# Kernel tuning notes

Hardware: AMD Instinct MI355X
Metric: run time of the kernel (lower is better)

## Reference

```python
import jax, jax.numpy as jnp
import numpy as np

E = 1024
H = 16
D = E // H
NUM_BUCKETS = 320
MAX_DISTANCE = 800


def _relative_positions_bucket(relative_positions):
    # relative_positions: int32 [T, S]
    num_buckets = NUM_BUCKETS // 2  # 160
    relative_buckets = (relative_positions > 0).astype(jnp.int32) * num_buckets
    rel = jnp.abs(relative_positions)
    max_exact = num_buckets // 2  # 80
    is_small = rel < max_exact
    rel_f = jnp.maximum(rel, 1).astype(jnp.float32)
    large = jnp.log(rel_f / max_exact) / np.log(MAX_DISTANCE / max_exact) * (num_buckets - max_exact)
    large = (max_exact + large).astype(jnp.int32)
    large = jnp.minimum(large, num_buckets - 1)
    relative_buckets = relative_buckets + jnp.where(is_small, rel, large)
    return relative_buckets


def setup_inputs() -> dict:
    key = jax.random.key(0)
    ks = jax.random.split(key, 12)
    B, T = 2, 2048
    s = 0.02
    return {
        "hidden_states": jax.random.normal(ks[0], (B, T, E), dtype=jnp.float32),
        "q_w": jax.random.normal(ks[1], (E, E), dtype=jnp.float32) * s,
        "q_b": jnp.zeros((E,), dtype=jnp.float32),
        "k_w": jax.random.normal(ks[2], (E, E), dtype=jnp.float32) * s,
        "k_b": jnp.zeros((E,), dtype=jnp.float32),
        "v_w": jax.random.normal(ks[3], (E, E), dtype=jnp.float32) * s,
        "v_b": jnp.zeros((E,), dtype=jnp.float32),
        "out_w": jax.random.normal(ks[4], (E, E), dtype=jnp.float32) * s,
        "out_b": jnp.zeros((E,), dtype=jnp.float32),
        "rel_embed": jax.random.normal(ks[5], (NUM_BUCKETS, H), dtype=jnp.float32) * s,
        "gru_const": jnp.ones((1, H, 1, 1), dtype=jnp.float32),
        "gru_w": jax.random.normal(ks[6], (8, D), dtype=jnp.float32) * s,
        "gru_b": jnp.zeros((8,), dtype=jnp.float32),
    }


def reference(hidden_states, q_w, q_b, k_w, k_b, v_w, v_b, out_w, out_b,
              rel_embed, gru_const, gru_w, gru_b):
    B, T, _ = hidden_states.shape
    scaling = D ** (-0.5)

    # --- relative position bias: [H, T, T] ---
    ctx = jnp.arange(T, dtype=jnp.int32)[:, None]
    mem = jnp.arange(T, dtype=jnp.int32)[None, :]
    buckets = _relative_positions_bucket(mem - ctx)          # [T, T]
    position_bias = rel_embed[buckets]                        # [T, T, H]
    position_bias = jnp.transpose(position_bias, (2, 0, 1))   # [H, T, T]

    # --- gate (gru_rel_pos): per (b, h, t) scalar ---
    gated = hidden_states.reshape(B, T, H, D).transpose(0, 2, 1, 3)  # [B,H,T,D]
    proj = jnp.einsum('bhtd,ed->bhte', gated, gru_w) + gru_b         # [B,H,T,8]
    proj = proj.reshape(B, H, T, 2, 4).sum(-1)                        # [B,H,T,2]
    gate = jax.nn.sigmoid(proj)
    gate_a = gate[..., 0:1]
    gate_b = gate[..., 1:2]
    gate_out = gate_a * (gate_b * gru_const - 1.0) + 2.0              # [B,H,T,1]
    gated_position_bias = gate_out * position_bias[None]              # [B,H,T,T]

    # --- attention (same math as F.multi_head_attention_forward eager path) ---
    q = (hidden_states @ q_w.T + q_b).reshape(B, T, H, D).transpose(0, 2, 1, 3) * scaling
    k = (hidden_states @ k_w.T + k_b).reshape(B, T, H, D).transpose(0, 2, 1, 3)
    v = (hidden_states @ v_w.T + v_b).reshape(B, T, H, D).transpose(0, 2, 1, 3)

    scores = jnp.einsum('bhtd,bhsd->bhts', q, k) + gated_position_bias
    attn = jax.nn.softmax(scores, axis=-1)
    ctx_out = jnp.einsum('bhts,bhsd->bhtd', attn, v)                  # [B,H,T,D]
    ctx_out = ctx_out.transpose(0, 2, 1, 3).reshape(B, T, E)
    return ctx_out @ out_w.T + out_b
```

## Files before the change

### kernel.cpp

```cpp
#include <hip/hip_runtime.h>
#include <hip/hip_bf16.h>
#include <math.h>

typedef __bf16 bf16;
typedef __bf16 bf16x4 __attribute__((ext_vector_type(4)));
typedef __bf16 bf16x8 __attribute__((ext_vector_type(8)));
typedef float  f32x4  __attribute__((ext_vector_type(4)));

#define T_SEQ 2048
#define E_DIM 1024
#define H_NUM 16
#define D_DIM 64
#define NDELTA 4095
#define LOG2E 1.4426950408889634f

__device__ __forceinline__ void gld16(const bf16* g, bf16* l) {
  __builtin_amdgcn_global_load_lds((__attribute__((address_space(1))) void*)(g),
                                   (__attribute__((address_space(3))) void*)(l), 16, 0, 0);
}

__global__ void cast_bf16_kernel(const float* __restrict__ src, bf16* __restrict__ dst, int n4) {
  int i = blockIdx.x * blockDim.x + threadIdx.x;
  if (i >= n4) return;
  const float4 v = reinterpret_cast<const float4*>(src)[i];
  bf16x4 o;
  o[0] = (bf16)v.x; o[1] = (bf16)v.y; o[2] = (bf16)v.z; o[3] = (bf16)v.w;
  reinterpret_cast<bf16x4*>(dst)[i] = o;
}

__global__ void cast_w_kernel(const float* __restrict__ q_w, const float* __restrict__ k_w,
                              const float* __restrict__ v_w, const float* __restrict__ o_w,
                              bf16* __restrict__ wcat, bf16* __restrict__ wob) {
  int i = blockIdx.x * 256 + threadIdx.x;
  int sel = blockIdx.y;
  const float* src = (sel == 0) ? q_w : (sel == 1) ? k_w : (sel == 2) ? v_w : o_w;
  bf16* dst = (sel < 3) ? (wcat + (size_t)sel * 1048576) : wob;
  const float4 v = reinterpret_cast<const float4*>(src)[i];
  bf16x4 o;
  o[0] = (bf16)v.x; o[1] = (bf16)v.y; o[2] = (bf16)v.z; o[3] = (bf16)v.w;
  reinterpret_cast<bf16x4*>(dst)[i] = o;
}

__global__ void pb_kernel(const float* __restrict__ rel_embed, float* __restrict__ pbt) {
  int dd = blockIdx.x * 64 + threadIdx.x;
  if (dd >= NDELTA) return;
  int delta = dd - (T_SEQ - 1);
  int bucket = (delta > 0) ? 160 : 0;
  int rel = abs(delta);
  int v;
  if (rel < 80) {
    v = rel;
  } else {
    float rf = (float)(rel < 1 ? 1 : rel);
    float lf = logf(rf / 80.0f) * (80.0f / 2.302585092994046f);
    int lg = 80 + (int)lf;
    v = lg < 159 ? lg : 159;
  }
  bucket += v;
#pragma unroll
  for (int h = 0; h < H_NUM; h++)
    pbt[h * NDELTA + dd] = rel_embed[bucket * H_NUM + h];
}

__global__ __launch_bounds__(256)
void gate_kernel(const float* __restrict__ hs, const float* __restrict__ gru_w,
                 const float* __restrict__ gru_b, const float* __restrict__ gconst,
                 float* __restrict__ gate)
{
  __shared__ float w[512];
  int tid = threadIdx.x;
  w[tid] = gru_w[tid];
  w[tid + 256] = gru_w[tid + 256];
  __syncthreads();
  int idx = blockIdx.x * 256 + tid;
  int h  = idx & 15;
  int bt = idx >> 4;
  const float* x = hs + (size_t)bt * E_DIM + h * D_DIM;
  float acc[8] = {0,0,0,0,0,0,0,0};
  for (int d = 0; d < 64; d += 4) {
    float4 xv = *(const float4*)&x[d];
#pragma unroll
    for (int e = 0; e < 8; e++) {
      acc[e] += xv.x * w[e*64+d] + xv.y * w[e*64+d+1]
              + xv.z * w[e*64+d+2] + xv.w * w[e*64+d+3];
    }
  }
  float p0 = acc[0]+acc[1]+acc[2]+acc[3] + gru_b[0]+gru_b[1]+gru_b[2]+gru_b[3];
  float p1 = acc[4]+acc[5]+acc[6]+acc[7] + gru_b[4]+gru_b[5]+gru_b[6]+gru_b[7];
  float ga = 1.0f / (1.0f + expf(-p0));
  float gb = 1.0f / (1.0f + expf(-p1));
  float g = (ga * (gb * gconst[h] - 1.0f) + 2.0f) * LOG2E;
  int bb = bt >> 11;
  int t  = bt & (T_SEQ - 1);
  gate[((size_t)(bb * H_NUM + h)) * T_SEQ + t] = g;
}

template<int MODE, int BM, int BN>
__global__ __launch_bounds__(256, 4)
void gemm4_kernel(const bf16* __restrict__ A, const bf16* __restrict__ W,
                  const float* __restrict__ b0, const float* __restrict__ b1,
                  const float* __restrict__ b2, float qalpha,
                  void* __restrict__ out0, void* __restrict__ out1, void* __restrict__ out2)
{
  constexpr int AM = BM / 32;
  constexpr int AN = BN / 32;
  __shared__ bf16 As[2][BM * 32];
  __shared__ bf16 Bs[2][BN * 32];
  const int tid  = threadIdx.x;
  const int lane = tid & 63;
  const int wave = tid >> 6;
  const int m0 = blockIdx.y * BM;
  const int n0 = blockIdx.x * BN;
  const int wm = (wave >> 1) * (BM / 2);
  const int wn = (wave & 1) * (BN / 2);
  const int qd = lane >> 4;
  const int lm = lane & 15;

  const int row4 = lane >> 2;
  const int col8 = (lane & 3) * 8;
  const bf16* gA0 = A + (size_t)(m0 + wave * (BM / 4) + row4) * 1024 + col8;
  const bf16* gB0 = W + (size_t)(n0 + wave * (BN / 4) + row4) * 1024 + col8;
  bf16* lA = (bf16*)As + wave * (BM / 4) * 32;
  bf16* lB = (bf16*)Bs + wave * (BN / 4) * 32;

  gld16(gA0, lA);
  if (BM == 128) gld16(gA0 + (size_t)16 * 1024, lA + 512);
  gld16(gB0, lB);
  if (BN == 128) gld16(gB0 + (size_t)16 * 1024, lB + 512);
  __syncthreads();

  f32x4 acc[AM][AN] = {};

  for (int k0 = 0; k0 < 1024; k0 += 32) {
    const int buf = (k0 >> 5) & 1;
    if (k0 + 32 < 1024) {
      bf16* lA1 = lA + (buf ^ 1) * (BM * 32);
      bf16* lB1 = lB + (buf ^ 1) * (BN * 32);
      gld16(gA0 + k0 + 32, lA1);
      if (BM == 128) gld16(gA0 + (size_t)16 * 1024 + k0 + 32, lA1 + 512);
      gld16(gB0 + k0 + 32, lB1);
      if (BN == 128) gld16(gB0 + (size_t)16 * 1024 + k0 + 32, lB1 + 512);
    }
    bf16x8 af[AM], bfr[AN];
#pragma unroll
    for (int i = 0; i < AM; i++)
      af[i]  = *(const bf16x8*)&As[buf][(wm + i * 16 + lm) * 32 + qd * 8];
#pragma unroll
    for (int i = 0; i < AN; i++)
      bfr[i] = *(const bf16x8*)&Bs[buf][(wn + i * 16 + lm) * 32 + qd * 8];
#pragma unroll
    for (int im = 0; im < AM; im++)
#pragma unroll
      for (int in = 0; in < AN; in++)
        acc[im][in] = __builtin_amdgcn_mfma_f32_16x16x32_bf16(af[im], bfr[in], acc[im][in], 0, 0, 0);
    __syncthreads();
  }

  const int seg = n0 >> 10;
  const float* bias = (MODE == 0) ? b0 : (seg == 0 ? b0 : (seg == 1 ? b1 : b2));
  const float alpha = (MODE == 1 && seg == 0) ? qalpha : 1.0f;

#pragma unroll
  for (int im = 0; im < AM; im++) {
#pragma unroll
    for (int in = 0; in < AN; in++) {
      const int n  = n0 + wn + in * 16 + lm;
      const int n1 = n & 1023;
      const float bv = bias[n1];
      const int mb = m0 + wm + im * 16 + qd * 4;
      if (MODE == 0) {
        float* o = (float*)out0;
#pragma unroll
        for (int r = 0; r < 4; r++)
          o[(size_t)(mb + r) * 1024 + n1] = acc[im][in][r] + bv;
      } else if (seg == 2) {
        const int bb = mb >> 11;
        const int t  = mb & 2047;
        bf16x4 pk;
#pragma unroll
        for (int r = 0; r < 4; r++) pk[r] = (bf16)(acc[im][in][r] + bv);
        *(bf16x4*)&((bf16*)out2)[((size_t)(bb * 1024 + n1)) * 2048 + t] = pk;
      } else {
        bf16* o = (bf16*)(seg == 0 ? out0 : out1);
#pragma unroll
        for (int r = 0; r < 4; r++)
          o[(size_t)(mb + r) * 1024 + n1] = (bf16)((acc[im][in][r] + bv) * alpha);
      }
    }
  }
}

#define LK 72
__global__ __launch_bounds__(256)
void attn3_kernel(const bf16* __restrict__ Qg, const bf16* __restrict__ Kg,
                  const bf16* __restrict__ Vtg, const float* __restrict__ gate,
                  const float* __restrict__ pbt, bf16* __restrict__ ctx)
{
  __shared__ bf16 Ks[2][64 * LK];
  __shared__ bf16 Vs[2][64 * LK];
  __shared__ bf16 Ps[4][32 * LK];
  __shared__ float pbs[2176];

  const int t0 = blockIdx.x * 128;
  const int h  = blockIdx.y;
  const int b  = blockIdx.z;
  const int tid  = threadIdx.x;
  const int lane = tid & 63;
  const int wave = tid >> 6;
  const int qd = lane >> 4;
  const int lm = lane & 15;

  for (int i = tid; i < 2176; i += 256) {
    int idx = i - t0 + 1920;
    pbs[i] = (idx >= 0 && idx < NDELTA) ? pbt[h * NDELTA + idx] : 0.0f;
  }

  bf16x8 qf[2][2];
  float g[2];
#pragma unroll
  for (int nb = 0; nb < 2; nb++) {
    const int q = t0 + wave * 32 + nb * 16 + lm;
    const bf16* qrow = Qg + (size_t)(b * T_SEQ + q) * E_DIM + h * D_DIM;
    qf[nb][0] = *(const bf16x8*)(qrow + qd * 8);
    qf[nb][1] = *(const bf16x8*)(qrow + 32 + qd * 8);
    g[nb] = gate[((size_t)(b * H_NUM + h)) * T_SEQ + q];
  }

  const int srow = tid >> 2;
  const int scol = (tid & 3) * 16;
  const bf16* kgp = Kg  + ((size_t)(b * T_SEQ) + srow) * E_DIM + h * D_DIM + scol;
  const bf16* vgp = Vtg + ((size_t)(b * 1024) + h * D_DIM + srow) * T_SEQ + scol;

  {
    bf16x8 a0 = *(const bf16x8*)kgp;
    bf16x8 a1 = *(const bf16x8*)(kgp + 8);
    bf16x8 c0 = *(const bf16x8*)vgp;
    bf16x8 c1 = *(const bf16x8*)(vgp + 8);
    *(bf16x8*)&Ks[0][srow * LK + scol]     = a0;
    *(bf16x8*)&Ks[0][srow * LK + scol + 8] = a1;
    *(bf16x8*)&Vs[0][srow * LK + scol]     = c0;
    *(bf16x8*)&Vs[0][srow * LK + scol + 8] = c1;
  }
  __syncthreads();

  f32x4 o[4][2] = {};
  float li[2] = {0.0f, 0.0f};
  bf16* psw = &Ps[wave][0];

  for (int it = 0; it < T_SEQ / 64; it++) {
    const int s0 = it * 64;
    const int buf = it & 1;
    const bool more = (it + 1 < T_SEQ / 64);
    bf16x8 nk0, nk1, nv0, nv1;
    if (more) {
      const bf16* kn = kgp + (size_t)(s0 + 64) * E_DIM;
      const bf16* vn = vgp + (s0 + 64);
      nk0 = *(const bf16x8*)kn; nk1 = *(const bf16x8*)(kn + 8);
      nv0 = *(const bf16x8*)vn; nv1 = *(const bf16x8*)(vn + 8);
    }

    bf16x8 kf[4][2];
#pragma unroll
    for (int mb = 0; mb < 4; mb++) {
      kf[mb][0] = *(const bf16x8*)&Ks[buf][(16 * mb + lm) * LK + qd * 8];
      kf[mb][1] = *(const bf16x8*)&Ks[buf][(16 * mb + lm) * LK + 32 + qd * 8];
    }
#pragma unroll
    for (int nb = 0; nb < 2; nb++) {
      f32x4 sc[4];
#pragma unroll
      for (int mb = 0; mb < 4; mb++) {
        f32x4 t = {};
        t = __builtin_amdgcn_mfma_f32_16x16x32_bf16(kf[mb][0], qf[nb][0], t, 0, 0, 0);
        t = __builtin_amdgcn_mfma_f32_16x16x32_bf16(kf[mb][1], qf[nb][1], t, 0, 0, 0);
        sc[mb] = t;
      }
      const int ib = s0 + 4 * qd + 127 - (wave * 32 + nb * 16 + lm);
      float rs = 0.0f;
#pragma unroll
      for (int mb = 0; mb < 4; mb++) {
        bf16x4 pk;
#pragma unroll
        for (int r = 0; r < 4; r++) {
          float p = __builtin_amdgcn_exp2f(sc[mb][r] + g[nb] * pbs[ib + 16 * mb + r]);
          rs += p;
          pk[r] = (bf16)p;
        }
        *(bf16x4*)&psw[(nb * 16 + lm) * LK + 16 * mb + 4 * qd] = pk;
      }
      li[nb] += rs;
    }
    bf16x8 pf[2][2];
#pragma unroll
    for (int nb = 0; nb < 2; nb++) {
      pf[nb][0] = *(const bf16x8*)&psw[(nb * 16 + lm) * LK + qd * 8];
      pf[nb][1] = *(const bf16x8*)&psw[(nb * 16 + lm) * LK + 32 + qd * 8];
    }
#pragma unroll
    for (int db = 0; db < 4; db++) {
      bf16x8 vf0 = *(const bf16x8*)&Vs[buf][(16 * db + lm) * LK + qd * 8];
      bf16x8 vf1 = *(const bf16x8*)&Vs[buf][(16 * db + lm) * LK + 32 + qd * 8];
#pragma unroll
      for (int nb = 0; nb < 2; nb++) {
        o[db][nb] = __builtin_amdgcn_mfma_f32_16x16x32_bf16(vf0, pf[nb][0], o[db][nb], 0, 0, 0);
        o[db][nb] = __builtin_amdgcn_mfma_f32_16x16x32_bf16(vf1, pf[nb][1], o[db][nb], 0, 0, 0);
      }
    }
    if (more) {
      *(bf16x8*)&Ks[buf ^ 1][srow * LK + scol]     = nk0;
      *(bf16x8*)&Ks[buf ^ 1][srow * LK + scol + 8] = nk1;
      *(bf16x8*)&Vs[buf ^ 1][srow * LK + scol]     = nv0;
      *(bf16x8*)&Vs[buf ^ 1][srow * LK + scol + 8] = nv1;
    }
    __syncthreads();
  }

#pragma unroll
  for (int nb = 0; nb < 2; nb++) {
    li[nb] += __shfl_xor(li[nb], 16);
    li[nb] += __shfl_xor(li[nb], 32);
  }
#pragma unroll
  for (int nb = 0; nb < 2; nb++) {
    const float inv = 1.0f / li[nb];
    const int q = t0 + wave * 32 + nb * 16 + lm;
    bf16* obase = ctx + (size_t)(b * T_SEQ + q) * E_DIM + h * D_DIM + 4 * qd;
#pragma unroll
    for (int db = 0; db < 4; db++) {
      bf16x4 ov;
      ov[0] = (bf16)(o[db][nb][0] * inv); ov[1] = (bf16)(o[db][nb][1] * inv);
      ov[2] = (bf16)(o[db][nb][2] * inv); ov[3] = (bf16)(o[db][nb][3] * inv);
      *(bf16x4*)&obase[16 * db] = ov;
    }
  }
}

extern "C" void kernel_launch(void* const* d_in, const int* in_sizes, int n_in,
                              void* d_out, int out_size, void* d_ws, size_t ws_size,
                              hipStream_t stream)
{
  const float* hs     = (const float*)d_in[0];
  const float* q_w    = (const float*)d_in[1];
  const float* q_b    = (const float*)d_in[2];
  const float* k_w    = (const float*)d_in[3];
  const float* k_b    = (const float*)d_in[4];
  const float* v_w    = (const float*)d_in[5];
  const float* v_b    = (const float*)d_in[6];
  const float* out_w  = (const float*)d_in[7];
  const float* out_b  = (const float*)d_in[8];
  const float* rel    = (const float*)d_in[9];
  const float* gconst = (const float*)d_in[10];
  const float* gru_w  = (const float*)d_in[11];
  const float* gru_b  = (const float*)d_in[12];

  char* p = (char*)d_ws;
  bf16* hsb  = (bf16*)p; p += (size_t)4096 * 1024 * 2;
  bf16* wcat = (bf16*)p; p += (size_t)3072 * 1024 * 2;
  bf16* wob  = (bf16*)p; p += (size_t)1024 * 1024 * 2;
  bf16* Qb   = (bf16*)p; p += (size_t)4096 * 1024 * 2;
  bf16* Kb   = (bf16*)p; p += (size_t)4096 * 1024 * 2;
  bf16* Vtb  = (bf16*)p; p += (size_t)2048 * 2048 * 2;
  bf16* ctxb = (bf16*)p; p += (size_t)4096 * 1024 * 2;
  float* gatep = (float*)p; p += (size_t)2 * H_NUM * T_SEQ * 4;
  float* pbt   = (float*)p; p += (size_t)H_NUM * NDELTA * 4;

  cast_bf16_kernel<<<4096, 256, 0, stream>>>(hs, hsb, 1048576);
  cast_w_kernel<<<dim3(1024, 4), 256, 0, stream>>>(q_w, k_w, v_w, out_w, wcat, wob);
  pb_kernel<<<64, 64, 0, stream>>>(rel, pbt);
  gate_kernel<<<256, 256, 0, stream>>>(hs, gru_w, gru_b, gconst, gatep);

  const float qalpha = 0.125f * LOG2E;
  gemm4_kernel<1, 64, 128><<<dim3(24, 64), 256, 0, stream>>>(
      hsb, wcat, q_b, k_b, v_b, qalpha, Qb, Kb, Vtb);

  attn3_kernel<<<dim3(T_SEQ / 128, H_NUM, 2), 256, 0, stream>>>(Qb, Kb, Vtb, gatep, pbt, ctxb);

  gemm4_kernel<0, 64, 64><<<dim3(16, 64), 256, 0, stream>>>(
      ctxb, wob, out_b, nullptr, nullptr, 1.0f, d_out, nullptr, nullptr);
}
```

Before: 229.9 us.

## Fuse prep kernels into one launch and rework attention bias and K/V buffering

Merges the four preprocessing kernels (input cast, weight cast, position-bias table, gate) into a single launch that dispatches on block index, removing three kernel launches. The attention kernel now stores the position bias as four shifted bf16 copies so each lane reads an aligned bf16x4 vector instead of four scalar floats. It also drops K/V double buffering in favour of a single buffer with two barriers per iteration, which cuts LDS use but serialises the refill against compute. The bf16 bias storage adds a small rounding error.

```diff
diff --git a/kernel.cpp b/kernel.cpp
--- a/kernel.cpp
+++ b/kernel.cpp
@@ -19,80 +19,82 @@
                                    (__attribute__((address_space(3))) void*)(l), 16, 0, 0);
 }
 
-__global__ void cast_bf16_kernel(const float* __restrict__ src, bf16* __restrict__ dst, int n4) {
-  int i = blockIdx.x * blockDim.x + threadIdx.x;
-  if (i >= n4) return;
-  const float4 v = reinterpret_cast<const float4*>(src)[i];
-  bf16x4 o;
-  o[0] = (bf16)v.x; o[1] = (bf16)v.y; o[2] = (bf16)v.z; o[3] = (bf16)v.w;
-  reinterpret_cast<bf16x4*>(dst)[i] = o;
-}
-
-__global__ void cast_w_kernel(const float* __restrict__ q_w, const float* __restrict__ k_w,
-                              const float* __restrict__ v_w, const float* __restrict__ o_w,
-                              bf16* __restrict__ wcat, bf16* __restrict__ wob) {
-  int i = blockIdx.x * 256 + threadIdx.x;
-  int sel = blockIdx.y;
-  const float* src = (sel == 0) ? q_w : (sel == 1) ? k_w : (sel == 2) ? v_w : o_w;
-  bf16* dst = (sel < 3) ? (wcat + (size_t)sel * 1048576) : wob;
-  const float4 v = reinterpret_cast<const float4*>(src)[i];
-  bf16x4 o;
-  o[0] = (bf16)v.x; o[1] = (bf16)v.y; o[2] = (bf16)v.z; o[3] = (bf16)v.w;
-  reinterpret_cast<bf16x4*>(dst)[i] = o;
-}
-
-__global__ void pb_kernel(const float* __restrict__ rel_embed, float* __restrict__ pbt) {
-  int dd = blockIdx.x * 64 + threadIdx.x;
-  if (dd >= NDELTA) return;
-  int delta = dd - (T_SEQ - 1);
-  int bucket = (delta > 0) ? 160 : 0;
-  int rel = abs(delta);
-  int v;
-  if (rel < 80) {
-    v = rel;
-  } else {
-    float rf = (float)(rel < 1 ? 1 : rel);
-    float lf = logf(rf / 80.0f) * (80.0f / 2.302585092994046f);
-    int lg = 80 + (int)lf;
-    v = lg < 159 ? lg : 159;
-  }
-  bucket += v;
-#pragma unroll
-  for (int h = 0; h < H_NUM; h++)
-    pbt[h * NDELTA + dd] = rel_embed[bucket * H_NUM + h];
-}
-
 __global__ __launch_bounds__(256)
-void gate_kernel(const float* __restrict__ hs, const float* __restrict__ gru_w,
-                 const float* __restrict__ gru_b, const float* __restrict__ gconst,
-                 float* __restrict__ gate)
+void prep_kernel(const float* __restrict__ hs,
+                 const float* __restrict__ q_w, const float* __restrict__ k_w,
+                 const float* __restrict__ v_w, const float* __restrict__ o_w,
+                 const float* __restrict__ rel_embed,
+                 const float* __restrict__ gru_w, const float* __restrict__ gru_b,
+                 const float* __restrict__ gconst,
+                 bf16* __restrict__ hsb, bf16* __restrict__ wcat, bf16* __restrict__ wob,
+                 float* __restrict__ pbt, float* __restrict__ gate)
 {
   __shared__ float w[512];
-  int tid = threadIdx.x;
-  w[tid] = gru_w[tid];
-  w[tid + 256] = gru_w[tid + 256];
-  __syncthreads();
-  int idx = blockIdx.x * 256 + tid;
-  int h  = idx & 15;
-  int bt = idx >> 4;
-  const float* x = hs + (size_t)bt * E_DIM + h * D_DIM;
-  float acc[8] = {0,0,0,0,0,0,0,0};
-  for (int d = 0; d < 64; d += 4) {
-    float4 xv = *(const float4*)&x[d];
-#pragma unroll
-    for (int e = 0; e < 8; e++) {
-      acc[e] += xv.x * w[e*64+d] + xv.y * w[e*64+d+1]
-              + xv.z * w[e*64+d+2] + xv.w * w[e*64+d+3];
-    }
-  }
-  float p0 = acc[0]+acc[1]+acc[2]+acc[3] + gru_b[0]+gru_b[1]+gru_b[2]+gru_b[3];
-  float p1 = acc[4]+acc[5]+acc[6]+acc[7] + gru_b[4]+gru_b[5]+gru_b[6]+gru_b[7];
-  float ga = 1.0f / (1.0f + expf(-p0));
-  float gb = 1.0f / (1.0f + expf(-p1));
-  float g = (ga * (gb * gconst[h] - 1.0f) + 2.0f) * LOG2E;
-  int bb = bt >> 11;
-  int t  = bt & (T_SEQ - 1);
-  gate[((size_t)(bb * H_NUM + h)) * T_SEQ + t] = g;
+  const int blk = blockIdx.x;
+  const int tid = threadIdx.x;
+
+  if (blk < 4096) {
+    int i = blk * 256 + tid;
+    const float4 v = reinterpret_cast<const float4*>(hs)[i];
+    bf16x4 o;
+    o[0] = (bf16)v.x; o[1] = (bf16)v.y; o[2] = (bf16)v.z; o[3] = (bf16)v.w;
+    reinterpret_cast<bf16x4*>(hsb)[i] = o;
+  } else if (blk < 8192) {
+    int bb = blk - 4096;
+    int sel = bb >> 10;
+    int i = (bb & 1023) * 256 + tid;
+    const float* src = (sel == 0) ? q_w : (sel == 1) ? k_w : (sel == 2) ? v_w : o_w;
+    bf16* dst = (sel < 3) ? (wcat + (size_t)sel * 1048576) : wob;
+    const float4 v = reinterpret_cast<const float4*>(src)[i];
+    bf16x4 o;
+    o[0] = (bf16)v.x; o[1] = (bf16)v.y; o[2] = (bf16)v.z; o[3] = (bf16)v.w;
+    reinterpret_cast<bf16x4*>(dst)[i] = o;
+  } else if (blk < 8208) {
+    int dd = (blk - 8192) * 256 + tid;
+    if (dd < NDELTA) {
+      int delta = dd - (T_SEQ - 1);
+      int bucket = (delta > 0) ? 160 : 0;
+      int rel = abs(delta);
+      int v;
+      if (rel < 80) {
+        v = rel;
+      } else {
+        float rf = (float)(rel < 1 ? 1 : rel);
+        float lf = logf(rf / 80.0f) * (80.0f / 2.302585092994046f);
+        int lg = 80 + (int)lf;
+        v = lg < 159 ? lg : 159;
+      }
+      bucket += v;
+#pragma unroll
+      for (int h = 0; h < H_NUM; h++)
+        pbt[h * NDELTA + dd] = rel_embed[bucket * H_NUM + h];
+    }
+  } else {
+    w[tid] = gru_w[tid];
+    w[tid + 256] = gru_w[tid + 256];
+    __syncthreads();
+    int idx = (blk - 8208) * 256 + tid;
+    int h  = idx & 15;
+    int bt = idx >> 4;
+    const float* x = hs + (size_t)bt * E_DIM + h * D_DIM;
+    float acc[8] = {0,0,0,0,0,0,0,0};
+    for (int d = 0; d < 64; d += 4) {
+      float4 xv = *(const float4*)&x[d];
+#pragma unroll
+      for (int e = 0; e < 8; e++) {
+        acc[e] += xv.x * w[e*64+d] + xv.y * w[e*64+d+1]
+                + xv.z * w[e*64+d+2] + xv.w * w[e*64+d+3];
+      }
+    }
+    float p0 = acc[0]+acc[1]+acc[2]+acc[3] + gru_b[0]+gru_b[1]+gru_b[2]+gru_b[3];
+    float p1 = acc[4]+acc[5]+acc[6]+acc[7] + gru_b[4]+gru_b[5]+gru_b[6]+gru_b[7];
+    float ga = 1.0f / (1.0f + expf(-p0));
+    float gb = 1.0f / (1.0f + expf(-p1));
+    float g = (ga * (gb * gconst[h] - 1.0f) + 2.0f) * LOG2E;
+    int bb = bt >> 11;
+    int t  = bt & (T_SEQ - 1);
+    gate[((size_t)(bb * H_NUM + h)) * T_SEQ + t] = g;
+  }
 }
 
 template<int MODE, int BM, int BN>
@@ -191,15 +193,16 @@
 }
 
 #define LK 72
+#define PSK 72
 __global__ __launch_bounds__(256)
-void attn3_kernel(const bf16* __restrict__ Qg, const bf16* __restrict__ Kg,
+void attn6_kernel(const bf16* __restrict__ Qg, const bf16* __restrict__ Kg,
                   const bf16* __restrict__ Vtg, const float* __restrict__ gate,
                   const float* __restrict__ pbt, bf16* __restrict__ ctx)
 {
-  __shared__ bf16 Ks[2][64 * LK];
-  __shared__ bf16 Vs[2][64 * LK];
-  __shared__ bf16 Ps[4][32 * LK];
-  __shared__ float pbs[2176];
+  __shared__ bf16 Ks[64 * LK];
+  __shared__ bf16 Vs[64 * LK];
+  __shared__ bf16 Ps[4][32 * PSK];
+  __shared__ bf16 pbs4[4][2176];
 
   const int t0 = blockIdx.x * 128;
   const int h  = blockIdx.y;
@@ -210,9 +213,12 @@
   const int qd = lane >> 4;
   const int lm = lane & 15;
 
-  for (int i = tid; i < 2176; i += 256) {
-    int idx = i - t0 + 1920;
-    pbs[i] = (idx >= 0 && idx < NDELTA) ? pbt[h * NDELTA + idx] : 0.0f;
+  for (int j = tid; j < 2176; j += 256) {
+#pragma unroll
+    for (int c4 = 0; c4 < 4; c4++) {
+      int gidx = j + c4 - 4 - t0 + 1920;
+      pbs4[c4][j] = (bf16)((gidx >= 0 && gidx < NDELTA) ? pbt[h * NDELTA + gidx] : 0.0f);
+    }
   }
 
   bf16x8 qf[2][2];
@@ -226,6 +232,9 @@
     g[nb] = gate[((size_t)(b * H_NUM + h)) * T_SEQ + q];
   }
 
+  const int c = (3 - lm) & 3;
+  const int ebase0 = 4 * qd + 131 - wave * 32 - lm - c;
+
   const int srow = tid >> 2;
   const int scol = (tid & 3) * 16;
   const bf16* kgp = Kg  + ((size_t)(b * T_SEQ) + srow) * E_DIM + h * D_DIM + scol;
@@ -236,10 +245,10 @@
     bf16x8 a1 = *(const bf16x8*)(kgp + 8);
     bf16x8 c0 = *(const bf16x8*)vgp;
     bf16x8 c1 = *(const bf16x8*)(vgp + 8);
-    *(bf16x8*)&Ks[0][srow * LK + scol]     = a0;
-    *(bf16x8*)&Ks[0][srow * LK + scol + 8] = a1;
-    *(bf16x8*)&Vs[0][srow * LK + scol]     = c0;
-    *(bf16x8*)&Vs[0][srow * LK + scol + 8] = c1;
+    *(bf16x8*)&Ks[srow * LK + scol]     = a0;
+    *(bf16x8*)&Ks[srow * LK + scol + 8] = a1;
+    *(bf16x8*)&Vs[srow * LK + scol]     = c0;
+    *(bf16x8*)&Vs[srow * LK + scol + 8] = c1;
   }
   __syncthreads();
 
@@ -249,7 +258,6 @@
 
   for (int it = 0; it < T_SEQ / 64; it++) {
     const int s0 = it * 64;
-    const int buf = it & 1;
     const bool more = (it + 1 < T_SEQ / 64);
     bf16x8 nk0, nk1, nv0, nv1;
     if (more) {
@@ -262,8 +270,8 @@
     bf16x8 kf[4][2];
 #pragma unroll
     for (int mb = 0; mb < 4; mb++) {
-      kf[mb][0] = *(const bf16x8*)&Ks[buf][(16 * mb + lm) * LK + qd * 8];
-      kf[mb][1] = *(const bf16x8*)&Ks[buf][(16 * mb + lm) * LK + 32 + qd * 8];
+      kf[mb][0] = *(const bf16x8*)&Ks[(16 * mb + lm) * LK + qd * 8];
+      kf[mb][1] = *(const bf16x8*)&Ks[(16 * mb + lm) * LK + 32 + qd * 8];
     }
 #pragma unroll
     for (int nb = 0; nb < 2; nb++) {
@@ -275,31 +283,32 @@
         t = __builtin_amdgcn_mfma_f32_16x16x32_bf16(kf[mb][1], qf[nb][1], t, 0, 0, 0);
         sc[mb] = t;
       }
-      const int ib = s0 + 4 * qd + 127 - (wave * 32 + nb * 16 + lm);
+      const int base = ebase0 + s0 - nb * 16;
       float rs = 0.0f;
 #pragma unroll
       for (int mb = 0; mb < 4; mb++) {
+        const bf16x4 bb4 = *(const bf16x4*)&pbs4[c][base + 16 * mb];
         bf16x4 pk;
 #pragma unroll
         for (int r = 0; r < 4; r++) {
-          float p = __builtin_amdgcn_exp2f(sc[mb][r] + g[nb] * pbs[ib + 16 * mb + r]);
+          float p = __builtin_amdgcn_exp2f(sc[mb][r] + g[nb] * (float)bb4[r]);
           rs += p;
           pk[r] = (bf16)p;
         }
-        *(bf16x4*)&psw[(nb * 16 + lm) * LK + 16 * mb + 4 * qd] = pk;
+        *(bf16x4*)&psw[(nb * 16 + lm) * PSK + 16 * mb + 4 * qd] = pk;
       }
       li[nb] += rs;
     }
     bf16x8 pf[2][2];
 #pragma unroll
     for (int nb = 0; nb < 2; nb++) {
-      pf[nb][0] = *(const bf16x8*)&psw[(nb * 16 + lm) * LK + qd * 8];
-      pf[nb][1] = *(const bf16x8*)&psw[(nb * 16 + lm) * LK + 32 + qd * 8];
+      pf[nb][0] = *(const bf16x8*)&psw[(nb * 16 + lm) * PSK + qd * 8];
+      pf[nb][1] = *(const bf16x8*)&psw[(nb * 16 + lm) * PSK + 32 + qd * 8];
     }
 #pragma unroll
     for (int db = 0; db < 4; db++) {
-      bf16x8 vf0 = *(const bf16x8*)&Vs[buf][(16 * db + lm) * LK + qd * 8];
-      bf16x8 vf1 = *(const bf16x8*)&Vs[buf][(16 * db + lm) * LK + 32 + qd * 8];
+      bf16x8 vf0 = *(const bf16x8*)&Vs[(16 * db + lm) * LK + qd * 8];
+      bf16x8 vf1 = *(const bf16x8*)&Vs[(16 * db + lm) * LK + 32 + qd * 8];
 #pragma unroll
       for (int nb = 0; nb < 2; nb++) {
         o[db][nb] = __builtin_amdgcn_mfma_f32_16x16x32_bf16(vf0, pf[nb][0], o[db][nb], 0, 0, 0);
@@ -307,12 +316,13 @@
       }
     }
     if (more) {
-      *(bf16x8*)&Ks[buf ^ 1][srow * LK + scol]     = nk0;
-      *(bf16x8*)&Ks[buf ^ 1][srow * LK + scol + 8] = nk1;
-      *(bf16x8*)&Vs[buf ^ 1][srow * LK + scol]     = nv0;
-      *(bf16x8*)&Vs[buf ^ 1][srow * LK + scol + 8] = nv1;
-    }
-    __syncthreads();
+      __syncthreads();
+      *(bf16x8*)&Ks[srow * LK + scol]     = nk0;
+      *(bf16x8*)&Ks[srow * LK + scol + 8] = nk1;
+      *(bf16x8*)&Vs[srow * LK + scol]     = nv0;
+      *(bf16x8*)&Vs[srow * LK + scol + 8] = nv1;
+      __syncthreads();
+    }
   }
 
 #pragma unroll
@@ -364,16 +374,14 @@
   float* gatep = (float*)p; p += (size_t)2 * H_NUM * T_SEQ * 4;
   float* pbt   = (float*)p; p += (size_t)H_NUM * NDELTA * 4;
 
-  cast_bf16_kernel<<<4096, 256, 0, stream>>>(hs, hsb, 1048576);
-  cast_w_kernel<<<dim3(1024, 4), 256, 0, stream>>>(q_w, k_w, v_w, out_w, wcat, wob);
-  pb_kernel<<<64, 64, 0, stream>>>(rel, pbt);
-  gate_kernel<<<256, 256, 0, stream>>>(hs, gru_w, gru_b, gconst, gatep);
+  prep_kernel<<<8464, 256, 0, stream>>>(hs, q_w, k_w, v_w, out_w, rel, gru_w, gru_b, gconst,
+                                        hsb, wcat, wob, pbt, gatep);
 
   const float qalpha = 0.125f * LOG2E;
   gemm4_kernel<1, 64, 128><<<dim3(24, 64), 256, 0, stream>>>(
       hsb, wcat, q_b, k_b, v_b, qalpha, Qb, Kb, Vtb);
 
-  attn3_kernel<<<dim3(T_SEQ / 128, H_NUM, 2), 256, 0, stream>>>(Qb, Kb, Vtb, gatep, pbt, ctxb);
+  attn6_kernel<<<dim3(T_SEQ / 128, H_NUM, 2), 256, 0, stream>>>(Qb, Kb, Vtb, gatep, pbt, ctxb);
 
   gemm4_kernel<0, 64, 64><<<dim3(16, 64), 256, 0, stream>>>(
       ctxb, wob, out_b, nullptr, nullptr, 1.0f, d_out, nullptr, nullptr);
```

Measured after the change: 245.0 us. 1.07x slower.
